# Kernel tuning notes

Hardware: AMD Instinct MI355X
Metric: run time of the kernel (lower is better)

The kernel has to match this reference:

```python
import jax, jax.numpy as jnp
import numpy as np

N_NODES = 100000
N_EDGES = 1600000
IN_DIM = 128
OUT_DIM = 10
N_GRAPHS = 512


def setup_inputs() -> dict:
    key = jax.random.key(0)
    ks = jax.random.split(key, 16)
    x = jax.random.normal(ks[0], (N_NODES, IN_DIM), dtype=jnp.float32)
    edge_index = jax.random.randint(ks[1], (2, N_EDGES), 0, N_NODES, dtype=jnp.int64)
    batch = jnp.sort(jax.random.randint(ks[2], (N_NODES,), 0, N_GRAPHS, dtype=jnp.int64))
    s = 0.1
    params = {
        'W1': jax.random.normal(ks[3], (IN_DIM, 32), dtype=jnp.float32) * s,
        'b1': jnp.zeros((32,), dtype=jnp.float32),
        'W2': jax.random.normal(ks[4], (32, 64), dtype=jnp.float32) * s,
        'b2': jnp.zeros((64,), dtype=jnp.float32),
        'W3': jax.random.normal(ks[5], (64, 128), dtype=jnp.float32) * s,
        'b3': jnp.zeros((128,), dtype=jnp.float32),
        'Wl1': jax.random.normal(ks[6], (128, 64), dtype=jnp.float32) * s,
        'bl1': jnp.zeros((64,), dtype=jnp.float32),
        'Wl2': jax.random.normal(ks[7], (64, OUT_DIM), dtype=jnp.float32) * s,
        'bl2': jnp.zeros((OUT_DIM,), dtype=jnp.float32),
    }
    return {'x': x, 'edge_index': edge_index, 'batch': batch, **params}


def _gcn_conv(x, src, dst, norm, W, b, n):
    # PyG GCNConv: out[i] = sum_j norm_ij * (x[j] @ W) + b, with self-loops folded into (src, dst).
    xw = x @ W                                   # [N, F_out]
    msg = xw[src] * norm[:, None]                # gather + scale  [E+N, F_out]
    return jax.ops.segment_sum(msg, dst, num_segments=n) + b


def reference(x, edge_index, batch, W1, b1, W2, b2, W3, b3, Wl1, bl1, Wl2, bl2):
    n = x.shape[0]
    loops = jnp.arange(n, dtype=edge_index.dtype)
    src = jnp.concatenate([edge_index[0], loops])  # j (source)
    dst = jnp.concatenate([edge_index[1], loops])  # i (target)
    # symmetric normalization D^{-1/2} (A+I) D^{-1/2}; degree at targets incl. self-loops
    deg = jax.ops.segment_sum(jnp.ones_like(dst, dtype=x.dtype), dst, num_segments=n)
    dinv = jnp.where(deg > 0, jax.lax.rsqrt(deg), 0.0)
    norm = dinv[src] * dinv[dst]
    # eval mode: dropout is identity
    h = jax.nn.relu(_gcn_conv(x, src, dst, norm, W1, b1, n))
    h = jax.nn.relu(_gcn_conv(h, src, dst, norm, W2, b2, n))
    h = _gcn_conv(h, src, dst, norm, W3, b3, n)
    g = jax.ops.segment_sum(h, batch, num_segments=N_GRAPHS)  # global_add_pool
    g = jax.nn.relu(g @ Wl1 + bl1)
    g = g @ Wl2 + bl2
    return jax.nn.log_softmax(g, axis=1)
```

## Files before the change

kernel.cpp:

```cpp
#include <hip/hip_runtime.h>
#include <hip/hip_bf16.h>
#include <math.h>
#include <type_traits>

#define NN 100000
#define NE 1600000
#define NG 512
#define NPB 128
#define NBUCK ((NN + NPB - 1) / NPB)
#define BCAP 3072
#define PBLOCKS 256
#define PTHREADS 1024

__device__ __forceinline__ float b2f(ushort u){ return __uint_as_float(((unsigned int)u)<<16); }
__device__ __forceinline__ ushort f2b(float f){
    __hip_bfloat16 h = __float2bfloat16(f);
    return *(ushort*)&h;
}
__device__ __forceinline__ float blo(unsigned int u){ return __uint_as_float(u<<16); }
__device__ __forceinline__ float bhi(unsigned int u){ return __uint_as_float(u & 0xffff0000u); }
__device__ __forceinline__ void acc4(float* a, uint2 u){
    a[0] += blo(u.x); a[1] += bhi(u.x); a[2] += blo(u.y); a[3] += bhi(u.y);
}

__global__ __launch_bounds__(PTHREADS) void part_kernel(const int* __restrict__ src, const int* __restrict__ dst,
                                                        int* __restrict__ bucket_cnt, int* __restrict__ recs, int e){
    __shared__ int hist[NBUCK];
    __shared__ int base_[NBUCK];
    int tid = threadIdx.x;
    for(int b=tid; b<NBUCK; b+=PTHREADS) hist[b]=0;
    __syncthreads();
    int per = (e + PBLOCKS - 1) / PBLOCKS;
    int lo = blockIdx.x * per;
    int hi = lo + per; if(hi > e) hi = e;
    for(int i=lo+tid; i<hi; i+=PTHREADS) atomicAdd(&hist[dst[i]>>7], 1);
    __syncthreads();
    for(int b=tid; b<NBUCK; b+=PTHREADS){
        int h = hist[b];
        base_[b] = h ? atomicAdd(&bucket_cnt[b], h) : 0;
        hist[b] = 0;
    }
    __syncthreads();
    for(int i=lo+tid; i<hi; i+=PTHREADS){
        int d = dst[i];
        int b = d >> 7;
        int rank = atomicAdd(&hist[b], 1);
        int pos  = base_[b] + rank;
        if(pos < BCAP) recs[(size_t)b*BCAP + pos] = ((d & 127) << 17) | src[i];
    }
}

__global__ __launch_bounds__(512) void bucket_csr_kernel(const int* __restrict__ recs, const int* __restrict__ bucket_cnt,
                                                         int* __restrict__ csr, int* __restrict__ row_start,
                                                         int* __restrict__ row_end, float* __restrict__ dinv, int n){
    __shared__ int sr[BCAP];
    __shared__ int h[NPB];
    __shared__ int pc[NPB];
    __shared__ int cur[NPB];
    int b = blockIdx.x, tid = threadIdx.x;
    int cnt = bucket_cnt[b]; if(cnt > BCAP) cnt = BCAP;
    for(int i=tid; i<cnt; i+=512) sr[i] = recs[(size_t)b*BCAP + i];
    if(tid < NPB) h[tid] = 0;
    __syncthreads();
    for(int i=tid; i<cnt; i+=512) atomicAdd(&h[sr[i]>>17], 1);
    __syncthreads();
    int hp = (tid < NPB) ? ((h[tid]+3)&~3) : 0;
    if(tid < NPB) pc[tid] = hp;
    __syncthreads();
    for(int off=1; off<NPB; off<<=1){
        int t = (tid>=off && tid<NPB) ? pc[tid-off] : 0;
        __syncthreads();
        if(tid<NPB) pc[tid] += t;
        __syncthreads();
    }
    if(tid < NPB){
        int excl = pc[tid] - hp;
        cur[tid] = excl;
        int node = b*NPB + tid;
        if(node < n){
            row_start[node] = b*BCAP + excl;
            row_end[node]   = b*BCAP + excl + h[tid];
            dinv[node] = rsqrtf((float)(h[tid] + 1));
        }
    }
    __syncthreads();
    for(int i=tid; i<cnt; i+=512){
        int rec = sr[i];
        int p = atomicAdd(&cur[rec>>17], 1);
        csr[(size_t)b*BCAP + p] = rec & 131071;
    }
}

template<int K, int NCOL, int RPT, bool BIAS, bool RELU, bool SCALE, bool BF16IN, bool BF16OUT>
__global__ __launch_bounds__(256) void gemm_kernel(const void* __restrict__ X_, const float* __restrict__ W,
                                                   const float* __restrict__ bias, const float* __restrict__ dinv,
                                                   void* __restrict__ Y_, int n){
    using TX = typename std::conditional<BF16IN, ushort, float>::type;
    const TX* __restrict__ X = (const TX*)X_;
    constexpr int CG = NCOL/4;
    constexpr int RT = 256/CG;
    constexpr int ROWS = RT*RPT;
    __shared__ float sW[K*NCOL];
    for(int i=threadIdx.x; i<K*NCOL/4; i+=256)
        ((float4*)sW)[i] = ((const float4*)W)[i];
    __syncthreads();
    int cg = threadIdx.x % CG;
    int rt = threadIdx.x / CG;
    int base = blockIdx.x*ROWS + rt*RPT;
    float acc[RPT][4];
    #pragma unroll
    for(int j=0;j<RPT;j++){ acc[j][0]=0.f; acc[j][1]=0.f; acc[j][2]=0.f; acc[j][3]=0.f; }
    const TX* xp[RPT];
    #pragma unroll
    for(int j=0;j<RPT;j++){
        int r = base+j; if(r>n-1) r=n-1;
        xp[j] = X + (size_t)r*K;
    }
    for(int k4=0;k4<K/4;k4++){
        float4 w0 = *(const float4*)&sW[(k4*4+0)*NCOL + cg*4];
        float4 w1 = *(const float4*)&sW[(k4*4+1)*NCOL + cg*4];
        float4 w2 = *(const float4*)&sW[(k4*4+2)*NCOL + cg*4];
        float4 w3 = *(const float4*)&sW[(k4*4+3)*NCOL + cg*4];
        #pragma unroll
        for(int j=0;j<RPT;j++){
            float4 xv;
            if constexpr(BF16IN){
                ushort4 xu = ((const ushort4*)xp[j])[k4];
                xv = make_float4(b2f(xu.x), b2f(xu.y), b2f(xu.z), b2f(xu.w));
            } else {
                xv = ((const float4*)xp[j])[k4];
            }
            acc[j][0] += xv.x*w0.x + xv.y*w1.x + xv.z*w2.x + xv.w*w3.x;
            acc[j][1] += xv.x*w0.y + xv.y*w1.y + xv.z*w2.y + xv.w*w3.y;
            acc[j][2] += xv.x*w0.z + xv.y*w1.z + xv.z*w2.z + xv.w*w3.z;
            acc[j][3] += xv.x*w0.w + xv.y*w1.w + xv.z*w2.w + xv.w*w3.w;
        }
    }
    float4 bv = make_float4(0.f,0.f,0.f,0.f);
    if constexpr(BIAS) bv = *(const float4*)&bias[cg*4];
    #pragma unroll
    for(int j=0;j<RPT;j++){
        int r = base+j;
        if(r<n){
            float4 o;
            o.x = acc[j][0]+bv.x; o.y = acc[j][1]+bv.y;
            o.z = acc[j][2]+bv.z; o.w = acc[j][3]+bv.w;
            if constexpr(RELU){
                o.x=fmaxf(o.x,0.f); o.y=fmaxf(o.y,0.f);
                o.z=fmaxf(o.z,0.f); o.w=fmaxf(o.w,0.f);
            }
            if constexpr(SCALE){
                float s = dinv[r];
                o.x*=s; o.y*=s; o.z*=s; o.w*=s;
            }
            if constexpr(BF16OUT){
                ushort4 u = make_ushort4(f2b(o.x), f2b(o.y), f2b(o.z), f2b(o.w));
                *(ushort4*)&((ushort*)Y_)[(size_t)r*NCOL + cg*4] = u;
            } else {
                *(float4*)&((float*)Y_)[(size_t)r*NCOL + cg*4] = o;
            }
        }
    }
}

template<int F, bool BIAS, bool RELU, bool POSTSCALE>
__global__ __launch_bounds__(256) void prop_kernel(const ushort* __restrict__ xin, ushort* __restrict__ xout,
                                                   const int* __restrict__ csr, const int* __restrict__ row_start,
                                                   const int* __restrict__ row_end, const float* __restrict__ dinv,
                                                   const float* __restrict__ bias, int n){
    constexpr int L = F/4;
    int gt  = blockIdx.x*256 + threadIdx.x;
    int node = gt / L;
    int f2   = gt & (L-1);
    if(node>=n) return;
    float di = dinv[node];
    const uint2* __restrict__ xw = ((const uint2*)xin) + f2;
    float a[4] = {0.f,0.f,0.f,0.f};
    float b[4] = {0.f,0.f,0.f,0.f};
    acc4(a, xw[(size_t)node*L]);
    int e  = row_start[node];
    int ee = row_end[node];
    for(; e+7<ee; e+=8){
        int4 c0 = *(const int4*)&csr[e];
        int4 c1 = *(const int4*)&csr[e+4];
        uint2 u0 = xw[(size_t)c0.x*L];
        uint2 u1 = xw[(size_t)c0.y*L];
        uint2 u2 = xw[(size_t)c0.z*L];
        uint2 u3 = xw[(size_t)c0.w*L];
        uint2 u4 = xw[(size_t)c1.x*L];
        uint2 u5 = xw[(size_t)c1.y*L];
        uint2 u6 = xw[(size_t)c1.z*L];
        uint2 u7 = xw[(size_t)c1.w*L];
        acc4(a,u0); acc4(b,u1); acc4(a,u2); acc4(b,u3);
        acc4(a,u4); acc4(b,u5); acc4(a,u6); acc4(b,u7);
    }
    if(e+3<ee){
        int4 c0 = *(const int4*)&csr[e];
        uint2 u0 = xw[(size_t)c0.x*L];
        uint2 u1 = xw[(size_t)c0.y*L];
        uint2 u2 = xw[(size_t)c0.z*L];
        uint2 u3 = xw[(size_t)c0.w*L];
        acc4(a,u0); acc4(b,u1); acc4(a,u2); acc4(b,u3);
        e += 4;
    }
    for(; e<ee; ++e) acc4(a, xw[(size_t)csr[e]*L]);
    float r0 = di*(a[0]+b[0]);
    float r1 = di*(a[1]+b[1]);
    float r2 = di*(a[2]+b[2]);
    float r3 = di*(a[3]+b[3]);
    if constexpr(BIAS){ r0 += bias[4*f2]; r1 += bias[4*f2+1]; r2 += bias[4*f2+2]; r3 += bias[4*f2+3]; }
    if constexpr(RELU){ r0=fmaxf(r0,0.f); r1=fmaxf(r1,0.f); r2=fmaxf(r2,0.f); r3=fmaxf(r3,0.f); }
    if constexpr(POSTSCALE){ r0*=di; r1*=di; r2*=di; r3*=di; }
    uint2 outu;
    outu.x = ((unsigned int)f2b(r1)<<16) | (unsigned int)f2b(r0);
    outu.y = ((unsigned int)f2b(r3)<<16) | (unsigned int)f2b(r2);
    ((uint2*)xout)[(size_t)node*L + f2] = outu;
}

__global__ __launch_bounds__(256) void pool_kernel(const ushort* __restrict__ p3, const int* __restrict__ batch,
                                                   float* __restrict__ pool, int* __restrict__ cnt, int n){
    __shared__ float4 red[256];
    int g = blockIdx.x;
    int lo=0, hi=n;
    while(lo<hi){ int mid=(lo+hi)>>1; if(batch[mid]<g) lo=mid+1; else hi=mid; }
    int start=lo;
    lo=start; hi=n;
    while(lo<hi){ int mid=(lo+hi)>>1; if(batch[mid]<g+1) lo=mid+1; else hi=mid; }
    int end=lo;
    int u = threadIdx.x & 15;
    int r = threadIdx.x >> 4;
    const uint2* __restrict__ pw = ((const uint2*)p3) + u;
    float a[4] = {0.f,0.f,0.f,0.f};
    for(int i=start+r; i<end; i+=16) acc4(a, pw[(size_t)i*16]);
    red[threadIdx.x] = make_float4(a[0],a[1],a[2],a[3]);
    __syncthreads();
    for(int s=128; s>=16; s>>=1){
        if(threadIdx.x < s){
            float4 o = red[threadIdx.x+s];
            red[threadIdx.x].x += o.x; red[threadIdx.x].y += o.y;
            red[threadIdx.x].z += o.z; red[threadIdx.x].w += o.w;
        }
        __syncthreads();
    }
    if(threadIdx.x < 16){
        float4 o = red[threadIdx.x];
        pool[g*64 + 4*threadIdx.x    ] = o.x;
        pool[g*64 + 4*threadIdx.x + 1] = o.y;
        pool[g*64 + 4*threadIdx.x + 2] = o.z;
        pool[g*64 + 4*threadIdx.x + 3] = o.w;
    }
    if(threadIdx.x==0) cnt[g] = end-start;
}

__global__ __launch_bounds__(128) void head_kernel(const float* __restrict__ pool, const int* __restrict__ cnt,
                                                   const float* __restrict__ W3, const float* __restrict__ b3,
                                                   const float* __restrict__ Wl1, const float* __restrict__ bl1,
                                                   const float* __restrict__ Wl2, const float* __restrict__ bl2,
                                                   float* __restrict__ out){
    __shared__ float sp[64];
    __shared__ float sg3[128];
    __shared__ float sh[64];
    __shared__ float sl[10];
    int g = blockIdx.x, t = threadIdx.x;
    if(t<64) sp[t] = pool[g*64+t];
    __syncthreads();
    float cf = (float)cnt[g];
    float a = cf*b3[t];
    #pragma unroll 8
    for(int k=0;k<64;k++) a += sp[k]*W3[k*128+t];
    sg3[t]=a; __syncthreads();
    if(t<64){
        float h = bl1[t];
        #pragma unroll 8
        for(int k=0;k<128;k++) h += sg3[k]*Wl1[k*64+t];
        sh[t] = fmaxf(h,0.f);
    }
    __syncthreads();
    if(t<10){
        float l = bl2[t];
        for(int k=0;k<64;k++) l += sh[k]*Wl2[k*10+t];
        sl[t]=l;
    }
    __syncthreads();
    if(t<10){
        float m=sl[0];
        for(int k=1;k<10;k++) m=fmaxf(m,sl[k]);
        float s=0.f;
        for(int k=0;k<10;k++) s+=expf(sl[k]-m);
        out[g*10+t] = sl[t]-m-logf(s);
    }
}

extern "C" void kernel_launch(void* const* d_in, const int* in_sizes, int n_in,
                              void* d_out, int out_size, void* d_ws, size_t ws_size,
                              hipStream_t stream){
    const float* x   = (const float*)d_in[0];
    const int*   ei  = (const int*)d_in[1];
    const int* batch = (const int*)d_in[2];
    const float* W1  = (const float*)d_in[3];
    const float* b1  = (const float*)d_in[4];
    const float* W2  = (const float*)d_in[5];
    const float* b2  = (const float*)d_in[6];
    const float* W3  = (const float*)d_in[7];
    const float* b3  = (const float*)d_in[8];
    const float* Wl1 = (const float*)d_in[9];
    const float* bl1 = (const float*)d_in[10];
    const float* Wl2 = (const float*)d_in[11];
    const float* bl2 = (const float*)d_in[12];
    const int n = NN, E = NE;
    const int* src = ei;
    const int* dst = ei + E;

    char* ws = (char*)d_ws;
    size_t off = 0;
    auto alloc = [&](size_t bytes)->char*{
        char* p = ws + off;
        off = (off + bytes + 255) & ~(size_t)255;
        return p;
    };
    int*    bucket_cnt = (int*)   alloc((size_t)NBUCK*4);
    float*  dinv       = (float*) alloc((size_t)n*4);
    int*    recs       = (int*)   alloc((size_t)NBUCK*BCAP*4);
    int*    csr        = (int*)   alloc((size_t)NBUCK*BCAP*4);
    int*    row_start  = (int*)   alloc((size_t)n*4);
    int*    row_end    = (int*)   alloc((size_t)n*4);
    ushort* y1         = (ushort*)alloc((size_t)n*32*2);
    ushort* h1y        = (ushort*)alloc((size_t)n*32*2);
    ushort* p2         = (ushort*)alloc((size_t)n*32*2);
    ushort* h2y        = (ushort*)alloc((size_t)n*64*2);
    ushort* p3         = (ushort*)alloc((size_t)n*64*2);
    float*  pool       = (float*) alloc((size_t)NG*64*4);
    int*    cnt        = (int*)   alloc((size_t)NG*4);

    hipMemsetAsync(bucket_cnt, 0, (size_t)NBUCK*4, stream);
    part_kernel<<<PBLOCKS,PTHREADS,0,stream>>>(src, dst, bucket_cnt, recs, E);
    bucket_csr_kernel<<<NBUCK,512,0,stream>>>(recs, bucket_cnt, csr, row_start, row_end, dinv, n);

    gemm_kernel<128,32,2,false,false,true,false,true><<<(n+63)/64,256,0,stream>>>(x, W1, nullptr, dinv, y1, n);
    prop_kernel<32,true,true,true><<<(n*8+255)/256,256,0,stream>>>(y1, h1y, csr, row_start, row_end, dinv, b1, n);
    prop_kernel<32,false,false,false><<<(n*8+255)/256,256,0,stream>>>(h1y, p2, csr, row_start, row_end, dinv, nullptr, n);
    gemm_kernel<32,64,4,true,true,true,true,true><<<(n+63)/64,256,0,stream>>>(p2, W2, b2, dinv, h2y, n);
    prop_kernel<64,false,false,false><<<(n*16+255)/256,256,0,stream>>>(h2y, p3, csr, row_start, row_end, dinv, nullptr, n);
    pool_kernel<<<NG,256,0,stream>>>(p3, batch, pool, cnt, n);
    head_kernel<<<NG,128,0,stream>>>(pool, cnt, W3, b3, Wl1, bl1, Wl2, bl2, (float*)d_out);
}
```

Before: 280.6 us.

## Fuse layer-2 propagation with W2 GEMM and layer-3 propagation with pooling

```diff
diff --git a/kernel.cpp b/kernel.cpp
--- a/kernel.cpp
+++ b/kernel.cpp
@@ -31,9 +31,19 @@
     for(int b=tid; b<NBUCK; b+=PTHREADS) hist[b]=0;
     __syncthreads();
     int per = (e + PBLOCKS - 1) / PBLOCKS;
+    per = (per + 3) & ~3;
     int lo = blockIdx.x * per;
     int hi = lo + per; if(hi > e) hi = e;
-    for(int i=lo+tid; i<hi; i+=PTHREADS) atomicAdd(&hist[dst[i]>>7], 1);
+    if(lo >= hi) return;
+    const int4* __restrict__ dst4 = (const int4*)dst;
+    const int4* __restrict__ src4 = (const int4*)src;
+    for(int i=lo/4+tid; i<hi/4; i+=PTHREADS){
+        int4 d = dst4[i];
+        atomicAdd(&hist[d.x>>7], 1);
+        atomicAdd(&hist[d.y>>7], 1);
+        atomicAdd(&hist[d.z>>7], 1);
+        atomicAdd(&hist[d.w>>7], 1);
+    }
     __syncthreads();
     for(int b=tid; b<NBUCK; b+=PTHREADS){
         int h = hist[b];
@@ -41,12 +51,18 @@
         hist[b] = 0;
     }
     __syncthreads();
-    for(int i=lo+tid; i<hi; i+=PTHREADS){
-        int d = dst[i];
-        int b = d >> 7;
-        int rank = atomicAdd(&hist[b], 1);
-        int pos  = base_[b] + rank;
-        if(pos < BCAP) recs[(size_t)b*BCAP + pos] = ((d & 127) << 17) | src[i];
+    for(int i=lo/4+tid; i<hi/4; i+=PTHREADS){
+        int4 d = dst4[i];
+        int4 s = src4[i];
+        int b0=d.x>>7, b1=d.y>>7, b2=d.z>>7, b3=d.w>>7;
+        int p0 = base_[b0] + atomicAdd(&hist[b0],1);
+        int p1 = base_[b1] + atomicAdd(&hist[b1],1);
+        int p2 = base_[b2] + atomicAdd(&hist[b2],1);
+        int p3 = base_[b3] + atomicAdd(&hist[b3],1);
+        if(p0 < BCAP) recs[(size_t)b0*BCAP + p0] = ((d.x & 127) << 17) | s.x;
+        if(p1 < BCAP) recs[(size_t)b1*BCAP + p1] = ((d.y & 127) << 17) | s.y;
+        if(p2 < BCAP) recs[(size_t)b2*BCAP + p2] = ((d.z & 127) << 17) | s.z;
+        if(p3 < BCAP) recs[(size_t)b3*BCAP + p3] = ((d.w & 127) << 17) | s.w;
     }
 }
 
@@ -217,42 +233,142 @@
     ((uint2*)xout)[(size_t)node*L + f2] = outu;
 }
 
-__global__ __launch_bounds__(256) void pool_kernel(const ushort* __restrict__ p3, const int* __restrict__ batch,
-                                                   float* __restrict__ pool, int* __restrict__ cnt, int n){
-    __shared__ float4 red[256];
-    int g = blockIdx.x;
-    int lo=0, hi=n;
-    while(lo<hi){ int mid=(lo+hi)>>1; if(batch[mid]<g) lo=mid+1; else hi=mid; }
-    int start=lo;
-    lo=start; hi=n;
-    while(lo<hi){ int mid=(lo+hi)>>1; if(batch[mid]<g+1) lo=mid+1; else hi=mid; }
-    int end=lo;
-    int u = threadIdx.x & 15;
-    int r = threadIdx.x >> 4;
-    const uint2* __restrict__ pw = ((const uint2*)p3) + u;
+__global__ __launch_bounds__(256) void prop_gemm_kernel(const ushort* __restrict__ xin, ushort* __restrict__ xout,
+                                                        const int* __restrict__ csr, const int* __restrict__ row_start,
+                                                        const int* __restrict__ row_end, const float* __restrict__ dinv,
+                                                        const float* __restrict__ W2, const float* __restrict__ b2, int n){
+    __shared__ float4 sW2v[32*16];
+    for(int i=threadIdx.x; i<512; i+=256) sW2v[i] = ((const float4*)W2)[i];
+    __syncthreads();
+    int gt  = blockIdx.x*256 + threadIdx.x;
+    int node = gt >> 3;
+    int og   = gt & 7;
+    if(node >= n) return;
+    float di = dinv[node];
+    const uint2* __restrict__ xw = ((const uint2*)xin) + og;
     float a[4] = {0.f,0.f,0.f,0.f};
-    for(int i=start+r; i<end; i+=16) acc4(a, pw[(size_t)i*16]);
-    red[threadIdx.x] = make_float4(a[0],a[1],a[2],a[3]);
-    __syncthreads();
-    for(int s=128; s>=16; s>>=1){
-        if(threadIdx.x < s){
-            float4 o = red[threadIdx.x+s];
-            red[threadIdx.x].x += o.x; red[threadIdx.x].y += o.y;
-            red[threadIdx.x].z += o.z; red[threadIdx.x].w += o.w;
+    float b[4] = {0.f,0.f,0.f,0.f};
+    acc4(a, xw[(size_t)node*8]);
+    int e  = row_start[node];
+    int ee = row_end[node];
+    for(; e+7<ee; e+=8){
+        int4 c0 = *(const int4*)&csr[e];
+        int4 c1 = *(const int4*)&csr[e+4];
+        uint2 u0 = xw[(size_t)c0.x*8];
+        uint2 u1 = xw[(size_t)c0.y*8];
+        uint2 u2 = xw[(size_t)c0.z*8];
+        uint2 u3 = xw[(size_t)c0.w*8];
+        uint2 u4 = xw[(size_t)c1.x*8];
+        uint2 u5 = xw[(size_t)c1.y*8];
+        uint2 u6 = xw[(size_t)c1.z*8];
+        uint2 u7 = xw[(size_t)c1.w*8];
+        acc4(a,u0); acc4(b,u1); acc4(a,u2); acc4(b,u3);
+        acc4(a,u4); acc4(b,u5); acc4(a,u6); acc4(b,u7);
+    }
+    if(e+3<ee){
+        int4 c0 = *(const int4*)&csr[e];
+        uint2 u0 = xw[(size_t)c0.x*8];
+        uint2 u1 = xw[(size_t)c0.y*8];
+        uint2 u2 = xw[(size_t)c0.z*8];
+        uint2 u3 = xw[(size_t)c0.w*8];
+        acc4(a,u0); acc4(b,u1); acc4(a,u2); acc4(b,u3);
+        e += 4;
+    }
+    for(; e<ee; ++e) acc4(a, xw[(size_t)csr[e]*8]);
+    float r[4];
+    r[0] = di*(a[0]+b[0]);
+    r[1] = di*(a[1]+b[1]);
+    r[2] = di*(a[2]+b[2]);
+    r[3] = di*(a[3]+b[3]);
+    float acc[8] = {0.f,0.f,0.f,0.f,0.f,0.f,0.f,0.f};
+    #pragma unroll
+    for(int k=0;k<32;k++){
+        float s = __shfl(r[k&3], k>>2, 8);
+        float4 wa = sW2v[k*16 + og*2];
+        float4 wb = sW2v[k*16 + og*2 + 1];
+        acc[0]+=s*wa.x; acc[1]+=s*wa.y; acc[2]+=s*wa.z; acc[3]+=s*wa.w;
+        acc[4]+=s*wb.x; acc[5]+=s*wb.y; acc[6]+=s*wb.z; acc[7]+=s*wb.w;
+    }
+    float4 ba = *(const float4*)&b2[og*8];
+    float4 bb = *(const float4*)&b2[og*8+4];
+    float o0 = di*fmaxf(acc[0]+ba.x, 0.f);
+    float o1 = di*fmaxf(acc[1]+ba.y, 0.f);
+    float o2 = di*fmaxf(acc[2]+ba.z, 0.f);
+    float o3 = di*fmaxf(acc[3]+ba.w, 0.f);
+    float o4 = di*fmaxf(acc[4]+bb.x, 0.f);
+    float o5 = di*fmaxf(acc[5]+bb.y, 0.f);
+    float o6 = di*fmaxf(acc[6]+bb.z, 0.f);
+    float o7 = di*fmaxf(acc[7]+bb.w, 0.f);
+    uint4 u;
+    u.x = ((unsigned int)f2b(o1)<<16) | (unsigned int)f2b(o0);
+    u.y = ((unsigned int)f2b(o3)<<16) | (unsigned int)f2b(o2);
+    u.z = ((unsigned int)f2b(o5)<<16) | (unsigned int)f2b(o4);
+    u.w = ((unsigned int)f2b(o7)<<16) | (unsigned int)f2b(o6);
+    ((uint4*)xout)[(size_t)node*8 + og] = u;
+}
+
+__global__ __launch_bounds__(256) void prop_pool_kernel(const ushort* __restrict__ xin,
+                                                        const int* __restrict__ csr, const int* __restrict__ row_start,
+                                                        const int* __restrict__ row_end, const float* __restrict__ dinv,
+                                                        const int* __restrict__ batch, float* __restrict__ pool, int n){
+    __shared__ float sp[16*64];
+    __shared__ int sg[16];
+    int base = blockIdx.x*16;
+    int tid = threadIdx.x;
+    int node = base + (tid >> 4);
+    int f2 = tid & 15;
+    if(tid < 16) sg[tid] = batch[base+tid];
+    float di = dinv[node];
+    const uint2* __restrict__ xw = ((const uint2*)xin) + f2;
+    float a[4] = {0.f,0.f,0.f,0.f};
+    float b[4] = {0.f,0.f,0.f,0.f};
+    acc4(a, xw[(size_t)node*16]);
+    int e  = row_start[node];
+    int ee = row_end[node];
+    for(; e+7<ee; e+=8){
+        int4 c0 = *(const int4*)&csr[e];
+        int4 c1 = *(const int4*)&csr[e+4];
+        uint2 u0 = xw[(size_t)c0.x*16];
+        uint2 u1 = xw[(size_t)c0.y*16];
+        uint2 u2 = xw[(size_t)c0.z*16];
+        uint2 u3 = xw[(size_t)c0.w*16];
+        uint2 u4 = xw[(size_t)c1.x*16];
+        uint2 u5 = xw[(size_t)c1.y*16];
+        uint2 u6 = xw[(size_t)c1.z*16];
+        uint2 u7 = xw[(size_t)c1.w*16];
+        acc4(a,u0); acc4(b,u1); acc4(a,u2); acc4(b,u3);
+        acc4(a,u4); acc4(b,u5); acc4(a,u6); acc4(b,u7);
+    }
+    if(e+3<ee){
+        int4 c0 = *(const int4*)&csr[e];
+        uint2 u0 = xw[(size_t)c0.x*16];
+        uint2 u1 = xw[(size_t)c0.y*16];
+        uint2 u2 = xw[(size_t)c0.z*16];
+        uint2 u3 = xw[(size_t)c0.w*16];
+        acc4(a,u0); acc4(b,u1); acc4(a,u2); acc4(b,u3);
+        e += 4;
+    }
+    for(; e<ee; ++e) acc4(a, xw[(size_t)csr[e]*16]);
+    float4 rv;
+    rv.x = di*(a[0]+b[0]);
+    rv.y = di*(a[1]+b[1]);
+    rv.z = di*(a[2]+b[2]);
+    rv.w = di*(a[3]+b[3]);
+    ((float4*)sp)[tid] = rv;
+    __syncthreads();
+    if(tid < 64){
+        int g0 = sg[0], g1 = sg[15];
+        for(int g=g0; g<=g1; ++g){
+            float s = 0.f;
+            #pragma unroll
+            for(int nl=0; nl<16; ++nl)
+                if(sg[nl]==g) s += sp[nl*64 + tid];
+            atomicAdd(&pool[g*64 + tid], s);
         }
-        __syncthreads();
-    }
-    if(threadIdx.x < 16){
-        float4 o = red[threadIdx.x];
-        pool[g*64 + 4*threadIdx.x    ] = o.x;
-        pool[g*64 + 4*threadIdx.x + 1] = o.y;
-        pool[g*64 + 4*threadIdx.x + 2] = o.z;
-        pool[g*64 + 4*threadIdx.x + 3] = o.w;
-    }
-    if(threadIdx.x==0) cnt[g] = end-start;
-}
-
-__global__ __launch_bounds__(128) void head_kernel(const float* __restrict__ pool, const int* __restrict__ cnt,
+    }
+}
+
+__global__ __launch_bounds__(128) void head_kernel(const float* __restrict__ pool, const int* __restrict__ batch, int n,
                                                    const float* __restrict__ W3, const float* __restrict__ b3,
                                                    const float* __restrict__ Wl1, const float* __restrict__ bl1,
                                                    const float* __restrict__ Wl2, const float* __restrict__ bl2,
@@ -264,7 +380,12 @@
     int g = blockIdx.x, t = threadIdx.x;
     if(t<64) sp[t] = pool[g*64+t];
     __syncthreads();
-    float cf = (float)cnt[g];
+    int lo=0, hi=n;
+    while(lo<hi){ int mid=(lo+hi)>>1; if(batch[mid]<g) lo=mid+1; else hi=mid; }
+    int start=lo;
+    lo=start; hi=n;
+    while(lo<hi){ int mid=(lo+hi)>>1; if(batch[mid]<g+1) lo=mid+1; else hi=mid; }
+    float cf = (float)(lo - start);
     float a = cf*b3[t];
     #pragma unroll 8
     for(int k=0;k<64;k++) a += sp[k]*W3[k*128+t];
@@ -326,21 +447,17 @@
     int*    row_end    = (int*)   alloc((size_t)n*4);
     ushort* y1         = (ushort*)alloc((size_t)n*32*2);
     ushort* h1y        = (ushort*)alloc((size_t)n*32*2);
-    ushort* p2         = (ushort*)alloc((size_t)n*32*2);
     ushort* h2y        = (ushort*)alloc((size_t)n*64*2);
-    ushort* p3         = (ushort*)alloc((size_t)n*64*2);
     float*  pool       = (float*) alloc((size_t)NG*64*4);
-    int*    cnt        = (int*)   alloc((size_t)NG*4);
 
     hipMemsetAsync(bucket_cnt, 0, (size_t)NBUCK*4, stream);
+    hipMemsetAsync(pool, 0, (size_t)NG*64*4, stream);
     part_kernel<<<PBLOCKS,PTHREADS,0,stream>>>(src, dst, bucket_cnt, recs, E);
     bucket_csr_kernel<<<NBUCK,512,0,stream>>>(recs, bucket_cnt, csr, row_start, row_end, dinv, n);
 
     gemm_kernel<128,32,2,false,false,true,false,true><<<(n+63)/64,256,0,stream>>>(x, W1, nullptr, dinv, y1, n);
     prop_kernel<32,true,true,true><<<(n*8+255)/256,256,0,stream>>>(y1, h1y, csr, row_start, row_end, dinv, b1, n);
-    prop_kernel<32,false,false,false><<<(n*8+255)/256,256,0,stream>>>(h1y, p2, csr, row_start, row_end, dinv, nullptr, n);
-    gemm_kernel<32,64,4,true,true,true,true,true><<<(n+63)/64,256,0,stream>>>(p2, W2, b2, dinv, h2y, n);
-    prop_kernel<64,false,false,false><<<(n*16+255)/256,256,0,stream>>>(h2y, p3, csr, row_start, row_end, dinv, nullptr, n);
-    pool_kernel<<<NG,256,0,stream>>>(p3, batch, pool, cnt, n);
-    head_kernel<<<NG,128,0,stream>>>(pool, cnt, W3, b3, Wl1, bl1, Wl2, bl2, (float*)d_out);
-}
+    prop_gemm_kernel<<<(n*8+255)/256,256,0,stream>>>(h1y, h2y, csr, row_start, row_end, dinv, W2, b2, n);
+    prop_pool_kernel<<<(n*16)/256,256,0,stream>>>(h2y, csr, row_start, row_end, dinv, batch, pool, n);
+    head_kernel<<<NG,128,0,stream>>>(pool, batch, n, W3, b3, Wl1, bl1, Wl2, bl2, (float*)d_out);
+}
```

After: 261.4 us. -6.9%, faster.
